# Optimization experiments

Measured on AMD Instinct MI355X. Metric: run time of the kernel, lower is better.

The kernel has to match this reference:

```python
import jax, jax.numpy as jnp
from jax import lax
import numpy as np

B = 32  # batch


def _conv(x, w, b, pad):
    # x: [B,Cin,H,W], w: [Cout,Cin,kh,kw], b: [Cout]
    y = lax.conv_general_dilated(x, w, window_strides=(1, 1), padding=pad,
                                 dimension_numbers=("NCHW", "OIHW", "NCHW"))
    return y + b[None, :, None, None]


def setup_inputs() -> dict:
    keys = jax.random.split(jax.random.key(0), 16)
    ki = iter(keys)
    f32 = jnp.float32

    def W(shape):
        return jax.random.normal(next(ki), shape, f32) * 0.05

    return {
        "x": jax.random.normal(next(ki), (B, 64, 64), f32),
        # 64 independent spatial convs per stage, each Conv2d(Cin,31,(64,3))
        "W1": W((64, 31, 1, 64, 3)),  "b1": jnp.zeros((64, 31), f32),
        "W2": W((64, 31, 31, 64, 3)), "b2": jnp.zeros((64, 31), f32),
        "W3": W((64, 31, 31, 64, 3)), "b3": jnp.zeros((64, 31), f32),
        # 2 edge spectral stacks: Conv(2,64,9)->ReLU->Conv(64,32,1)->ReLU->Conv(32,1,5)
        "We1a": W((2, 64, 2, 9, 9)),  "be1a": jnp.zeros((2, 64), f32),
        "We1b": W((2, 32, 64, 1, 1)), "be1b": jnp.zeros((2, 32), f32),
        "We1c": W((2, 1, 32, 5, 5)),  "be1c": jnp.zeros((2, 1), f32),
        # 29 interior spectral stacks: Conv(3,64,9)->ReLU->Conv(64,32,1)->ReLU->Conv(32,1,5)
        "We2a": W((29, 64, 3, 9, 9)),  "be2a": jnp.zeros((29, 64), f32),
        "We2b": W((29, 32, 64, 1, 1)), "be2b": jnp.zeros((29, 32), f32),
        "We2c": W((29, 1, 32, 5, 5)),  "be2c": jnp.zeros((29, 1), f32),
    }


def _spatial(inp, Ws, bs):
    # inp: [B,Cin,64,64]; Ws: [64,31,Cin,64,3]; bs: [64,31]
    def one(w, b):
        return jax.nn.relu(_conv(inp, w, b, [(0, 0), (1, 1)]))  # [B,31,1,64]
    rows = jax.vmap(one)(Ws, bs)            # [64,B,31,1,64]; row i = output line i
    return jnp.transpose(rows[:, :, :, 0, :], (1, 2, 0, 3))  # [B,31,64,64]


def _spectral(xin, wa, ba, wb, bb, wc, bc):
    h = jax.nn.relu(_conv(xin, wa, ba, [(4, 4), (4, 4)]))
    h = jax.nn.relu(_conv(h, wb, bb, [(0, 0), (0, 0)]))
    return _conv(h, wc, bc, [(2, 2), (2, 2)])[:, 0]  # [B,64,64]


def reference(x, W1, b1, W2, b2, W3, b3,
              We1a, be1a, We1b, be1b, We1c, be1c,
              We2a, be2a, We2b, be2b, We2c, be2c):
    xb = x[:, None]                         # [B,1,64,64]
    s1 = _spatial(xb, W1, b1)               # [B,31,64,64]
    s2 = _spatial(s1, W2, b2)
    s3 = _spatial(s2, W3, b3)

    # edge bands 0 and 30 use 2-channel slices
    edge_in = jnp.stack([s3[:, 0:2], s3[:, 29:31]])   # [2,B,2,64,64]
    edge = jax.vmap(_spectral)(edge_in, We1a, be1a, We1b, be1b, We1c, be1c)  # [2,B,64,64]

    # interior bands 1..29 use sliding 3-channel slices
    idx = jnp.arange(29)[:, None] + jnp.arange(3)[None, :]  # [29,3]
    mid_in = jnp.transpose(s3[:, idx], (1, 0, 2, 3, 4))     # [29,B,3,64,64]
    mid = jax.vmap(_spectral)(mid_in, We2a, be2a, We2b, be2b, We2c, be2c)  # [29,B,64,64]

    recon = jnp.concatenate(
        [edge[0][:, None], jnp.transpose(mid, (1, 0, 2, 3)), edge[1][:, None]], axis=1)
    out = s3 + recon                        # [B,31,64,64]
    # torch: .transpose(3,1).transpose(2,1) == permute(0,2,3,1)
    return jnp.transpose(out, (0, 2, 3, 1))  # [B,64,64,31]
```

## Files before the change

kernel.cpp:

```cpp
#include <hip/hip_runtime.h>
#include <hip/hip_bf16.h>
#include <stdint.h>

typedef unsigned short u16;
typedef unsigned int   u32;
typedef __attribute__((ext_vector_type(8))) short bf16x8;
typedef __attribute__((ext_vector_type(4))) float f32x4;

__device__ __forceinline__ float us2f(u16 u){ return __uint_as_float(((u32)u)<<16); }
__device__ __forceinline__ float lo2f(u32 w){ return __uint_as_float(w<<16); }
__device__ __forceinline__ float hi2f(u32 w){ return __uint_as_float(w & 0xffff0000u); }
__device__ __forceinline__ u16 f2us(float f){
  u32 u = __float_as_uint(f);
  u32 r = (u + 0x7FFFu + ((u>>16)&1u)) >> 16;
  return (u16)r;
}
__device__ __forceinline__ u32 pk2(float a, float b){ return (u32)f2us(a) | ((u32)f2us(b)<<16); }

__global__ __launch_bounds__(256) void k_prep_x(const float* __restrict__ x, u16* __restrict__ xT){
  __shared__ float tile[64][65];
  const int b = blockIdx.x, t = threadIdx.x;
  #pragma unroll
  for (int q=0;q<4;q++){
    int idx = q*256 + t, r = idx>>4, w4 = (idx&15)*4;
    float4 v = *(const float4*)&x[((size_t)b*64 + r)*64 + w4];
    tile[r][w4]=v.x; tile[r][w4+1]=v.y; tile[r][w4+2]=v.z; tile[r][w4+3]=v.w;
  }
  __syncthreads();
  #pragma unroll
  for (int q=0;q<2;q++){
    int idx = q*256 + t, w = idx>>3, rc = idx&7;
    uint4 o;
    o.x = pk2(tile[rc*8+0][w], tile[rc*8+1][w]);
    o.y = pk2(tile[rc*8+2][w], tile[rc*8+3][w]);
    o.z = pk2(tile[rc*8+4][w], tile[rc*8+5][w]);
    o.w = pk2(tile[rc*8+6][w], tile[rc*8+7][w]);
    *(uint4*)&xT[((size_t)b*64 + w)*64 + rc*8] = o;
  }
}

__global__ __launch_bounds__(256) void k_prep_w(const float* __restrict__ W,
        u16* __restrict__ Wp, int CI){
  __shared__ float rowW[5952];
  const int h = blockIdx.x, i = blockIdx.y, t = threadIdx.x;
  for (int idx=t; idx<1488; idx+=256){
    int o = idx/48, j4 = (idx - o*48)*4;
    float4 v = *(const float4*)&W[ (((size_t)h*31 + o)*CI + i)*192 + j4 ];
    *(float4*)&rowW[o*192 + j4] = v;
  }
  __syncthreads();
  for (int idx=t; idx<768; idx+=256){
    int dw = idx>>8, rem = idx&255, o = rem>>3, rc = rem&7;
    uint4 ov = {0,0,0,0};
    if (o < 31){
      const float* s = &rowW[o*192 + dw];
      ov.x = pk2(s[(rc*8+0)*3], s[(rc*8+1)*3]);
      ov.y = pk2(s[(rc*8+2)*3], s[(rc*8+3)*3]);
      ov.z = pk2(s[(rc*8+4)*3], s[(rc*8+5)*3]);
      ov.w = pk2(s[(rc*8+6)*3], s[(rc*8+7)*3]);
    }
    *(uint4*)&Wp[ ((((size_t)h*CI + i)*3 + dw)*32 + o)*64 + rc*8 ] = ov;
  }
}

__global__ __launch_bounds__(256) void k_tr(const u16* __restrict__ in, u16* __restrict__ outp){
  __shared__ u16 tile[64*72];
  const int b = blockIdx.x, o = blockIdx.y, t = threadIdx.x;
  const uint4* src = (const uint4*)(in + ((size_t)b*31 + o)*4096);
  #pragma unroll
  for (int q=0;q<2;q++){
    int idx = q*256 + t, hh = idx>>3, u = idx&7;
    *(uint4*)&tile[hh*72 + ((u ^ ((hh>>3)&7))*8)] = src[idx];
  }
  __syncthreads();
  u16* dst = outp + ((size_t)b*31 + o)*4096;
  #pragma unroll
  for (int q=0;q<2;q++){
    int idx = q*256 + t, w = idx>>3, hc = (idx&7)*8;
    u32 ow[4];
    #pragma unroll
    for (int j=0;j<4;j++){
      int h0 = hc + j*2, h1 = h0 + 1;
      u16 a = tile[h0*72 + (((w>>3) ^ ((h0>>3)&7))*8) + (w&7)];
      u16 bb= tile[h1*72 + (((w>>3) ^ ((h1>>3)&7))*8) + (w&7)];
      ow[j] = (u32)a | ((u32)bb<<16);
    }
    uint4 ov = {ow[0], ow[1], ow[2], ow[3]};
    *(uint4*)&dst[(size_t)w*64 + hc] = ov;
  }
}

__global__ __launch_bounds__(256) void k_spatial2(const u16* __restrict__ inT_g,
        const u16* __restrict__ Wp, const float* __restrict__ bias,
        float* __restrict__ outF, u16* __restrict__ outT, int CI, int mode){
  __shared__ __align__(16) u16 inT[2][66*72];
  const int t    = threadIdx.x;
  const int wv   = t>>6;
  const int lane = t&63;
  const int l15  = lane&15;
  const int quad = lane>>4;
  const int wg  = blockIdx.x;
  const int xcd = wg & 7;
  const int li  = wg >> 3;
  const int hg  = xcd*2 + (li>>5);
  const int b   = li & 31;
  const int h   = hg*4 + wv;

  if (t < 72){
    inT[0][t] = 0; inT[0][65*72 + t] = 0;
    inT[1][t] = 0; inT[1][65*72 + t] = 0;
  }

  f32x4 acc[2][4];
  #pragma unroll
  for (int n=0;n<2;n++)
    #pragma unroll
    for (int ms=0;ms<4;ms++) acc[n][ms] = (f32x4){0.f,0.f,0.f,0.f};

  const uint4* srcb = (const uint4*)(inT_g + (size_t)b*CI*4096);
  const u16*   wrow = Wp + (size_t)h*CI*3*32*64;

  uint4 pf[2];
  #pragma unroll
  for (int q=0;q<2;q++) pf[q] = srcb[q*256 + t];
  bf16x8 bA[2][3][2], bB[2][3][2];
  #pragma unroll
  for (int dw=0;dw<3;dw++)
    #pragma unroll
    for (int n=0;n<2;n++)
      #pragma unroll
      for (int kh=0;kh<2;kh++)
        bA[kh][dw][n] = *(const bf16x8*)&wrow[(dw*32 + n*16 + l15)*64 + kh*32 + quad*8];

  auto body = [&](bf16x8 (&bcur)[2][3][2], bf16x8 (&bnext)[2][3][2], int i){
    u16* L = inT[i&1];
    #pragma unroll
    for (int q=0;q<2;q++){
      int idx = q*256 + t, row = idx>>3, ch = idx&7;
      *(uint4*)&L[(row+1)*72 + ch*8] = pf[q];
    }
    int inext = (i+1 < CI) ? (i+1) : (CI-1);
    const uint4* src = srcb + (size_t)inext*512;
    #pragma unroll
    for (int q=0;q<2;q++) pf[q] = src[q*256 + t];
    const u16* wbase = wrow + (size_t)inext*3*32*64;
    #pragma unroll
    for (int dw=0;dw<3;dw++)
      #pragma unroll
      for (int n=0;n<2;n++)
        #pragma unroll
        for (int kh=0;kh<2;kh++)
          bnext[kh][dw][n] = *(const bf16x8*)&wbase[(dw*32 + n*16 + l15)*64 + kh*32 + quad*8];
    asm volatile("s_waitcnt lgkmcnt(0)" ::: "memory");
    __builtin_amdgcn_s_barrier();
    __builtin_amdgcn_sched_barrier(0);
    #pragma unroll
    for (int kh=0; kh<2; kh++){
      #pragma unroll
      for (int dw=0; dw<3; dw++){
        bf16x8 afr[4];
        #pragma unroll
        for (int ms=0;ms<4;ms++)
          afr[ms] = *(const bf16x8*)&L[(ms*16 + l15 + dw)*72 + kh*32 + quad*8];
        #pragma unroll
        for (int n=0;n<2;n++)
          #pragma unroll
          for (int ms=0;ms<4;ms++)
            acc[n][ms] = __builtin_amdgcn_mfma_f32_16x16x32_bf16(afr[ms], bcur[kh][dw][n], acc[n][ms], 0,0,0);
      }
    }
  };

  int i = 0;
  while (true){
    body(bA, bB, i); if (++i >= CI) break;
    body(bB, bA, i); if (++i >= CI) break;
  }

  #pragma unroll
  for (int n=0;n<2;n++){
    int o = n*16 + l15;
    if (o < 31){
      float bv = bias[h*31 + o];
      if (mode == 0){
        #pragma unroll
        for (int ms=0;ms<4;ms++){
          size_t base = (((size_t)b*31 + o)*64 + h)*64 + ms*16 + quad*4;
          #pragma unroll
          for (int reg=0;reg<4;reg++)
            outF[base + reg] = fmaxf(acc[n][ms][reg] + bv, 0.f);
        }
      } else {
        #pragma unroll
        for (int ms=0;ms<4;ms++){
          uint2 pw;
          pw.x = pk2(fmaxf(acc[n][ms][0] + bv, 0.f), fmaxf(acc[n][ms][1] + bv, 0.f));
          pw.y = pk2(fmaxf(acc[n][ms][2] + bv, 0.f), fmaxf(acc[n][ms][3] + bv, 0.f));
          *(uint2*)&outT[ (((size_t)b*31 + o)*64 + h)*64 + ms*16 + quad*4 ] = pw;
        }
      }
    }
  }
}

__global__ __launch_bounds__(256) void k_prep(
    const float* __restrict__ We1a, const float* __restrict__ We2a,
    const float* __restrict__ We1b, const float* __restrict__ We2b,
    u16* __restrict__ waP, u16* __restrict__ wbP){
  int t = blockIdx.x*256 + threadIdx.x;
  if (t < 17856){
    int g = t/576, rem = t - g*576, dx = rem>>6, c = rem&63;
    int C; const float* wa;
    if (g==0)      { C=2; wa = We1a; }
    else if (g==30){ C=2; wa = We1a + 64*2*81; }
    else           { C=3; wa = We2a + (size_t)(g-1)*64*3*81; }
    const float* wrow = wa + (size_t)c*C*81;
    u16* dst = waP + ((size_t)(g*9 + dx)*64 + c)*40;
    int Kr = C*9;
    for (int k=0;k<40;k++){
      u16 v = 0;
      if (k < Kr) v = f2us(wrow[k*9 + dx]);
      dst[k] = v;
    }
  } else if (t < 17856 + 992){
    int u = t - 17856; int g = u>>5, c2 = u&31;
    const float* wb;
    if (g==0)      wb = We1b;
    else if (g==30) wb = We1b + 32*64;
    else            wb = We2b + (size_t)(g-1)*32*64;
    u16* dst = wbP + ((size_t)g*32 + c2)*72;
    for (int k=0;k<64;k++) dst[k] = f2us(wb[c2*64 + k]);
    for (int k=64;k<72;k++) dst[k] = 0;
  }
}

__global__ __launch_bounds__(256) void k_spec_ab(
    const float* __restrict__ s3,
    const u16* __restrict__ waP, const u16* __restrict__ wbP,
    const float* __restrict__ be1a, const float* __restrict__ be1b,
    const float* __restrict__ be2a, const float* __restrict__ be2b,
    u16* __restrict__ hb, int g0){
  __shared__ __align__(16) unsigned char smem[36864];
  u16* colT = (u16*)smem;
  u16* haT  = (u16*)smem;
  u16* hbL  = (u16*)smem;

  const int t = threadIdx.x;
  const int yo = blockIdx.x, b = blockIdx.y;
  const int gl = blockIdx.z;
  const int g  = g0 + gl;
  const int y0 = yo*4;
  const int wv = t>>6, lane = t&63, l15 = lane&15, quad = lane>>4;

  int C, cb; const float *ba, *bb;
  if (g==0)      { C=2; cb=0;  ba=be1a;           bb=be1b;        }
  else if (g==30){ C=2; cb=29; ba=be1a+64;        bb=be1b+32;     }
  else           { C=3; cb=g-1; ba=be2a+(size_t)(g-1)*64; bb=be2b+(size_t)(g-1)*32; }

  {
    uint4 z = {0,0,0,0};
    uint4* c4 = (uint4*)colT;
    #pragma unroll
    for (int j=0;j<6;j++){ int idx = j*256 + t; if (idx < 1440) c4[idx] = z; }
  }
  __syncthreads();

  for (int idx=t; idx<576; idx+=256){
    int i = idx/192, rem = idx-192*i;
    int x4 = rem/12, yext = rem - x4*12;
    int yrow = y0 + yext - 4;
    if (i < C && yrow >= 0 && yrow < 64){
      float4 v = *(const float4*)&s3[ (((size_t)b*31 + cb + i)*64 + yrow)*64 + x4*4 ];
      u16 q0=f2us(v.x), q1=f2us(v.y), q2=f2us(v.z), q3=f2us(v.w);
      #pragma unroll
      for (int yl=0; yl<4; yl++){
        int dy = yext - yl;
        if (dy >= 0 && dy < 9){
          int k = i*9 + dy;
          int base = (yl*72 + x4*4 + 4)*40 + k;
          colT[base      ] = q0;
          colT[base + 40 ] = q1;
          colT[base + 80 ] = q2;
          colT[base + 120] = q3;
        }
      }
    }
  }
  __syncthreads();

  f32x4 acc[4][4];
  #pragma unroll
  for (int yl=0;yl<4;yl++)
    #pragma unroll
    for (int nf=0;nf<4;nf++) acc[yl][nf] = (f32x4){0.f,0.f,0.f,0.f};

  const u16* waPg = waP + (size_t)g*9*64*40;
  #pragma unroll
  for (int dx=0; dx<9; dx++){
    bf16x8 af[4];
    #pragma unroll
    for (int yl=0;yl<4;yl++)
      af[yl] = *(const bf16x8*)&colT[(yl*72 + wv*16 + l15 + dx)*40 + quad*8];
    #pragma unroll
    for (int nf=0;nf<4;nf++){
      bf16x8 bfr = *(const bf16x8*)&waPg[(dx*64 + nf*16 + l15)*40 + quad*8];
      #pragma unroll
      for (int yl=0;yl<4;yl++)
        acc[yl][nf] = __builtin_amdgcn_mfma_f32_16x16x32_bf16(af[yl], bfr, acc[yl][nf], 0,0,0);
    }
  }
  __syncthreads();

  #pragma unroll
  for (int nf=0;nf<4;nf++){
    float bav = ba[nf*16 + l15];
    #pragma unroll
    for (int yl=0;yl<4;yl++){
      int px = yl*64 + wv*16 + quad*4;
      #pragma unroll
      for (int reg=0;reg<4;reg++)
        haT[(px+reg)*72 + nf*16 + l15] = f2us(fmaxf(acc[yl][nf][reg] + bav, 0.f));
    }
  }
  __syncthreads();

  bf16x8 a2[2][4];
  #pragma unroll
  for (int kh=0; kh<2; kh++)
    #pragma unroll
    for (int j=0;j<4;j++)
      a2[kh][j] = *(const bf16x8*)&haT[((wv*4+j)*16 + l15)*72 + kh*32 + quad*8];
  __syncthreads();

  const u16* wb_g = wbP + (size_t)g*32*72;
  f32x4 acc2[4][2];
  #pragma unroll
  for (int j=0;j<4;j++){ acc2[j][0] = (f32x4){0.f,0.f,0.f,0.f}; acc2[j][1] = (f32x4){0.f,0.f,0.f,0.f}; }
  #pragma unroll
  for (int kh=0; kh<2; kh++){
    #pragma unroll
    for (int nf=0;nf<2;nf++){
      bf16x8 b2 = *(const bf16x8*)&wb_g[(nf*16 + l15)*72 + kh*32 + quad*8];
      #pragma unroll
      for (int j=0;j<4;j++)
        acc2[j][nf] = __builtin_amdgcn_mfma_f32_16x16x32_bf16(a2[kh][j], b2, acc2[j][nf], 0,0,0);
    }
  }
  #pragma unroll
  for (int nf=0;nf<2;nf++){
    float bbv = bb[nf*16 + l15];
    #pragma unroll
    for (int j=0;j<4;j++){
      int px = (wv*4+j)*16 + quad*4;
      uint2 pw;
      pw.x = pk2(fmaxf(acc2[j][nf][0] + bbv, 0.f), fmaxf(acc2[j][nf][1] + bbv, 0.f));
      pw.y = pk2(fmaxf(acc2[j][nf][2] + bbv, 0.f), fmaxf(acc2[j][nf][3] + bbv, 0.f));
      *(uint2*)&hbL[(nf*16+l15)*296 + px] = pw;
    }
  }
  __syncthreads();

  {
    int c2 = t>>3, xq = t&7;
    size_t base = (((size_t)gl*32 + b)*32 + c2)*4096 + (size_t)yo*256 + xq*32;
    #pragma unroll
    for (int q=0;q<4;q++)
      *(uint4*)&hb[base + q*8] = *(const uint4*)&hbL[c2*296 + xq*32 + q*8];
  }
}

__global__ __launch_bounds__(256) void k_spec_c(
    const u16* __restrict__ hb, const float* __restrict__ We1c, const float* __restrict__ be1c,
    const float* __restrict__ We2c, const float* __restrict__ be2c,
    float* __restrict__ rec, int g0){
  __shared__ __align__(16) unsigned char smemC[58368 + 3200];
  u16*   hbT  = (u16*)smemC;
  float* wcL  = (float*)(smemC + 58368);
  float* redc = (float*)smemC;
  const int t  = threadIdx.x;
  const int y0 = blockIdx.x*8;
  const int b  = blockIdx.y;
  const int gl = blockIdx.z;
  const int g  = g0 + gl;
  const float *wc, *bc;
  if (g==0)      { wc = We1c;             bc = be1c;       }
  else if (g==30){ wc = We1c + 800;       bc = be1c + 1;   }
  else           { wc = We2c + (g-1)*800; bc = be2c + (g-1); }

  for (int idx=t; idx<384; idx+=256){
    int c2 = idx/12, row = idx - c2*12;
    u32* d32 = (u32*)&hbT[(size_t)(c2*12 + row)*76];
    d32[0]  = 0;
    d32[33] = 0;
    u32* di = d32 + 1;
    int yg = y0 - 2 + row;
    if (yg >= 0 && yg < 64){
      const uint4* srcp = (const uint4*)&hb[ (((size_t)gl*32 + b)*32 + c2)*4096 + (size_t)yg*64 ];
      #pragma unroll
      for (int q=0;q<8;q++){
        uint4 v = srcp[q];
        di[q*4+0]=v.x; di[q*4+1]=v.y; di[q*4+2]=v.z; di[q*4+3]=v.w;
      }
    } else {
      #pragma unroll
      for (int q=0;q<32;q++) di[q] = 0;
    }
  }
  for (int idx=t; idx<800; idx+=256) wcL[idx] = wc[idx];
  __syncthreads();

  const int xt = t&7, yq = (t>>3)&7, cqt = t>>6;
  const int x0 = xt*8;
  float acc[8];
  #pragma unroll
  for (int p=0;p<8;p++) acc[p]=0.f;
  for (int c2 = cqt*8; c2 < cqt*8+8; c2++){
    #pragma unroll
    for (int dy=0;dy<5;dy++){
      const uint2* hp = (const uint2*)&hbT[(c2*12 + yq+dy)*76 + x0];
      uint2 v0 = hp[0], v1 = hp[1], v2 = hp[2];
      float h[12];
      h[0]=lo2f(v0.x); h[1]=hi2f(v0.x); h[2]=lo2f(v0.y); h[3]=hi2f(v0.y);
      h[4]=lo2f(v1.x); h[5]=hi2f(v1.x); h[6]=lo2f(v1.y); h[7]=hi2f(v1.y);
      h[8]=lo2f(v2.x); h[9]=hi2f(v2.x); h[10]=lo2f(v2.y); h[11]=hi2f(v2.y);
      #pragma unroll
      for (int dx=0;dx<5;dx++){
        float wv = wcL[c2*25 + dy*5 + dx];
        #pragma unroll
        for (int p=0;p<8;p++) acc[p] = fmaf(h[p+dx], wv, acc[p]);
      }
    }
  }
  __syncthreads();
  int slot = yq*8 + xt;
  if (cqt >= 2){
    #pragma unroll
    for (int p=0;p<8;p++) redc[((cqt-2)*64 + slot)*8 + p] = acc[p];
  }
  __syncthreads();
  if (cqt < 2){
    #pragma unroll
    for (int p=0;p<8;p++) acc[p] += redc[(cqt*64 + slot)*8 + p];
  }
  __syncthreads();
  if (cqt == 1){
    #pragma unroll
    for (int p=0;p<8;p++) redc[slot*8 + p] = acc[p];
  }
  __syncthreads();
  if (cqt == 0){
    float bcv = bc[0];
    size_t base = (((size_t)g*32 + b)*64 + (y0+yq))*64 + x0;
    #pragma unroll
    for (int p=0;p<8;p++) rec[base+p] = acc[p] + redc[slot*8 + p] + bcv;
  }
}

__global__ __launch_bounds__(256) void k_final(const float* __restrict__ s3,
        const float* __restrict__ rec, float* __restrict__ out){
  __shared__ float tile[31][65];
  const int t = threadIdx.x;
  const int y = blockIdx.x & 63;
  const int b = blockIdx.x >> 6;
  for (int idx=t; idx<1984; idx+=256){
    int o = idx>>6, x = idx&63;
    tile[o][x] = s3[ (((size_t)b*31+o)*64 + y)*64 + x ]
               + rec[ (((size_t)o*32+b)*64 + y)*64 + x ];
  }
  __syncthreads();
  size_t base = ((size_t)b*4096 + (size_t)y*64)*31;
  for (int idx=t; idx<1984; idx+=256){
    int x = idx/31, o = idx-31*x;
    out[base+idx] = tile[o][x];
  }
}

extern "C" void kernel_launch(void* const* d_in, const int* in_sizes, int n_in,
                              void* d_out, int out_size, void* d_ws, size_t ws_size,
                              hipStream_t stream){
  const float* x    = (const float*)d_in[0];
  const float* W1   = (const float*)d_in[1];
  const float* b1   = (const float*)d_in[2];
  const float* W2   = (const float*)d_in[3];
  const float* b2   = (const float*)d_in[4];
  const float* W3   = (const float*)d_in[5];
  const float* b3   = (const float*)d_in[6];
  const float* We1a = (const float*)d_in[7];
  const float* be1a = (const float*)d_in[8];
  const float* We1b = (const float*)d_in[9];
  const float* be1b = (const float*)d_in[10];
  const float* We1c = (const float*)d_in[11];
  const float* be1c = (const float*)d_in[12];
  const float* We2a = (const float*)d_in[13];
  const float* be2a = (const float*)d_in[14];
  const float* We2b = (const float*)d_in[15];
  const float* be2b = (const float*)d_in[16];
  const float* We2c = (const float*)d_in[17];
  const float* be2c = (const float*)d_in[18];
  float* out = (float*)d_out;

  char* ws = (char*)d_ws;
  float* s3  = (float*)(ws);
  u16*   Wp  = (u16*)(ws + 16777216);
  u16*   xT  = (u16*)(ws + 44040192);
  float* rec = (float*)(ws + 16777216);
  u16*   hb  = (u16*)(ws + 33030144);

  u16* bufA = (u16*)((char*)d_out);
  u16* bufB = (u16*)((char*)d_out + 8126464);
  u16* waP = (u16*)((char*)d_out);
  u16* wbP = (u16*)((char*)d_out + 1440000);

  dim3 bs(256);
  dim3 gsp(512), gtr(32,31);
  k_prep_x<<<dim3(32),bs,0,stream>>>(x, xT);
  k_prep_w<<<dim3(64,1),bs,0,stream>>>(W1, Wp, 1);
  k_spatial2<<<gsp,bs,0,stream>>>(xT,  Wp, b1, nullptr, bufA, 1, 1);
  k_tr<<<gtr,bs,0,stream>>>(bufA, bufB);
  k_prep_w<<<dim3(64,31),bs,0,stream>>>(W2, Wp, 31);
  k_spatial2<<<gsp,bs,0,stream>>>(bufB, Wp, b2, nullptr, bufA, 31, 1);
  k_tr<<<gtr,bs,0,stream>>>(bufA, bufB);
  k_prep_w<<<dim3(64,31),bs,0,stream>>>(W3, Wp, 31);
  k_spatial2<<<gsp,bs,0,stream>>>(bufB, Wp, b3, s3, nullptr, 31, 0);

  k_prep<<<dim3(74),bs,0,stream>>>(We1a, We2a, We1b, We2b, waP, wbP);

  int batch = 8;
  if (ws_size > 33030144ull){
    size_t m = (ws_size - 33030144ull) / 8388608ull;
    if (m < 1) m = 1;
    if (m > 8) m = 8;
    batch = (int)m;
  }
  for (int g0=0; g0<31; g0+=batch){
    int c = 31 - g0; if (c > batch) c = batch;
    k_spec_ab<<<dim3(16,32,c),bs,0,stream>>>(s3, waP, wbP, be1a, be1b, be2a, be2b, hb, g0);
    k_spec_c <<<dim3(8,32,c),bs,0,stream>>>(hb, We1c,be1c,We2c,be2c, rec, g0);
  }
  k_final<<<dim3(2048),bs,0,stream>>>(s3, rec, out);
}
```

Before: 994.5 us.

## Split spatial conv work per wave over half-width tiles with private LDS

Each workgroup of the spatial conv kernel now covers 2 output rows times 2 half-width column halves, one per wave, and the grid doubles to 1024 blocks. Each wave stages its own 34-row halo slice in a private LDS buffer, so the block-wide barrier and the double-buffered weight prefetch go away. Weight fragments are now loaded per kh right before use, and launch bounds request 4 blocks per CU. The aim is more parallelism and occupancy with fewer registers and less sync. In exchange, weight loads are exposed, adjacent waves reload overlapping halo rows, and the kernel relies on LDS reads completing without an explicit wait between the store and the MFMA loads.

```diff
diff --git a/kernel.cpp b/kernel.cpp
--- a/kernel.cpp
+++ b/kernel.cpp
@@ -90,10 +90,10 @@
   }
 }
 
-__global__ __launch_bounds__(256) void k_spatial2(const u16* __restrict__ inT_g,
+__global__ __launch_bounds__(256, 4) void k_spatial2(const u16* __restrict__ inT_g,
         const u16* __restrict__ Wp, const float* __restrict__ bias,
         float* __restrict__ outF, u16* __restrict__ outT, int CI, int mode){
-  __shared__ __align__(16) u16 inT[2][66*72];
+  __shared__ __align__(16) u16 S[4][34*72];
   const int t    = threadIdx.x;
   const int wv   = t>>6;
   const int lane = t&63;
@@ -102,79 +102,79 @@
   const int wg  = blockIdx.x;
   const int xcd = wg & 7;
   const int li  = wg >> 3;
-  const int hg  = xcd*2 + (li>>5);
+  const int hp  = li >> 5;
   const int b   = li & 31;
-  const int h   = hg*4 + wv;
-
-  if (t < 72){
-    inT[0][t] = 0; inT[0][65*72 + t] = 0;
-    inT[1][t] = 0; inT[1][65*72 + t] = 0;
-  }
-
-  f32x4 acc[2][4];
+  const int h   = xcd*8 + hp*2 + (wv&1);
+  const int wh  = wv >> 1;
+  const int w0  = wh*32;
+
+  u16* L = S[wv];
+
+  f32x4 acc[2][2];
   #pragma unroll
   for (int n=0;n<2;n++)
     #pragma unroll
-    for (int ms=0;ms<4;ms++) acc[n][ms] = (f32x4){0.f,0.f,0.f,0.f};
+    for (int ms=0;ms<2;ms++) acc[n][ms] = (f32x4){0.f,0.f,0.f,0.f};
 
   const uint4* srcb = (const uint4*)(inT_g + (size_t)b*CI*4096);
   const u16*   wrow = Wp + (size_t)h*CI*3*32*64;
 
-  uint4 pf[2];
-  #pragma unroll
-  for (int q=0;q<2;q++) pf[q] = srcb[q*256 + t];
-  bf16x8 bA[2][3][2], bB[2][3][2];
-  #pragma unroll
-  for (int dw=0;dw<3;dw++)
-    #pragma unroll
-    for (int n=0;n<2;n++)
-      #pragma unroll
-      for (int kh=0;kh<2;kh++)
-        bA[kh][dw][n] = *(const bf16x8*)&wrow[(dw*32 + n*16 + l15)*64 + kh*32 + quad*8];
-
-  auto body = [&](bf16x8 (&bcur)[2][3][2], bf16x8 (&bnext)[2][3][2], int i){
-    u16* L = inT[i&1];
-    #pragma unroll
-    for (int q=0;q<2;q++){
-      int idx = q*256 + t, row = idx>>3, ch = idx&7;
-      *(uint4*)&L[(row+1)*72 + ch*8] = pf[q];
-    }
-    int inext = (i+1 < CI) ? (i+1) : (CI-1);
-    const uint4* src = srcb + (size_t)inext*512;
-    #pragma unroll
-    for (int q=0;q<2;q++) pf[q] = src[q*256 + t];
-    const u16* wbase = wrow + (size_t)inext*3*32*64;
-    #pragma unroll
-    for (int dw=0;dw<3;dw++)
-      #pragma unroll
-      for (int n=0;n<2;n++)
+  uint4 pf[5];
+  const uint4 zz = {0,0,0,0};
+
+  auto issue_pf = [&](int ch){
+    const uint4* src = srcb + (size_t)ch*512;
+    #pragma unroll
+    for (int k=0;k<4;k++){
+      int c = lane + 64*k, row = c>>3, cn = c&7;
+      int gw = w0 - 1 + row;
+      pf[k] = zz;
+      if (gw >= 0 && gw < 64) pf[k] = src[gw*8 + cn];
+    }
+    {
+      int c = 256 + lane, row = c>>3, cn = c&7;
+      int gw = w0 - 1 + row;
+      pf[4] = zz;
+      if (lane < 16 && gw >= 0 && gw < 64) pf[4] = src[gw*8 + cn];
+    }
+  };
+
+  issue_pf(0);
+
+  for (int i=0;i<CI;i++){
+    #pragma unroll
+    for (int k=0;k<4;k++){
+      int c = lane + 64*k, row = c>>3, cn = c&7;
+      *(uint4*)&L[row*72 + cn*8] = pf[k];
+    }
+    if (lane < 16){
+      int c = 256 + lane, row = c>>3, cn = c&7;
+      *(uint4*)&L[row*72 + cn*8] = pf[4];
+    }
+    if (i+1 < CI) issue_pf(i+1);
+
+    const u16* wbase = wrow + (size_t)i*6144;
+    #pragma unroll
+    for (int kh=0; kh<2; kh++){
+      bf16x8 bfrk[3][2];
+      #pragma unroll
+      for (int dw=0;dw<3;dw++)
         #pragma unroll
-        for (int kh=0;kh<2;kh++)
-          bnext[kh][dw][n] = *(const bf16x8*)&wbase[(dw*32 + n*16 + l15)*64 + kh*32 + quad*8];
-    asm volatile("s_waitcnt lgkmcnt(0)" ::: "memory");
-    __builtin_amdgcn_s_barrier();
-    __builtin_amdgcn_sched_barrier(0);
-    #pragma unroll
-    for (int kh=0; kh<2; kh++){
+        for (int n=0;n<2;n++)
+          bfrk[dw][n] = *(const bf16x8*)&wbase[(dw*32 + n*16 + l15)*64 + kh*32 + quad*8];
       #pragma unroll
       for (int dw=0; dw<3; dw++){
-        bf16x8 afr[4];
+        bf16x8 afr[2];
         #pragma unroll
-        for (int ms=0;ms<4;ms++)
+        for (int ms=0;ms<2;ms++)
           afr[ms] = *(const bf16x8*)&L[(ms*16 + l15 + dw)*72 + kh*32 + quad*8];
         #pragma unroll
         for (int n=0;n<2;n++)
           #pragma unroll
-          for (int ms=0;ms<4;ms++)
-            acc[n][ms] = __builtin_amdgcn_mfma_f32_16x16x32_bf16(afr[ms], bcur[kh][dw][n], acc[n][ms], 0,0,0);
+          for (int ms=0;ms<2;ms++)
+            acc[n][ms] = __builtin_amdgcn_mfma_f32_16x16x32_bf16(afr[ms], bfrk[dw][n], acc[n][ms], 0,0,0);
       }
     }
-  };
-
-  int i = 0;
-  while (true){
-    body(bA, bB, i); if (++i >= CI) break;
-    body(bB, bA, i); if (++i >= CI) break;
   }
 
   #pragma unroll
@@ -184,19 +184,19 @@
       float bv = bias[h*31 + o];
       if (mode == 0){
         #pragma unroll
-        for (int ms=0;ms<4;ms++){
-          size_t base = (((size_t)b*31 + o)*64 + h)*64 + ms*16 + quad*4;
+        for (int ms=0;ms<2;ms++){
+          size_t base = (((size_t)b*31 + o)*64 + h)*64 + w0 + ms*16 + quad*4;
           #pragma unroll
           for (int reg=0;reg<4;reg++)
             outF[base + reg] = fmaxf(acc[n][ms][reg] + bv, 0.f);
         }
       } else {
         #pragma unroll
-        for (int ms=0;ms<4;ms++){
+        for (int ms=0;ms<2;ms++){
           uint2 pw;
           pw.x = pk2(fmaxf(acc[n][ms][0] + bv, 0.f), fmaxf(acc[n][ms][1] + bv, 0.f));
           pw.y = pk2(fmaxf(acc[n][ms][2] + bv, 0.f), fmaxf(acc[n][ms][3] + bv, 0.f));
-          *(uint2*)&outT[ (((size_t)b*31 + o)*64 + h)*64 + ms*16 + quad*4 ] = pw;
+          *(uint2*)&outT[ (((size_t)b*31 + o)*64 + h)*64 + w0 + ms*16 + quad*4 ] = pw;
         }
       }
     }
@@ -512,7 +512,7 @@
   u16* wbP = (u16*)((char*)d_out + 1440000);
 
   dim3 bs(256);
-  dim3 gsp(512), gtr(32,31);
+  dim3 gsp(1024), gtr(32,31);
   k_prep_x<<<dim3(32),bs,0,stream>>>(x, xT);
   k_prep_w<<<dim3(64,1),bs,0,stream>>>(W1, Wp, 1);
   k_spatial2<<<gsp,bs,0,stream>>>(xT,  Wp, b1, nullptr, bufA, 1, 1);
```

Result: slower. 1.132 ms (+13.9%).

## Retile spatial conv blocks to 2 rows × 2 batches per workgroup

Applied to the files above, without the earlier changes.

Each workgroup of k_spatial2 now covers 2 output rows for 2 batch samples instead of 4 rows for 1 sample. It stages two input images per channel in a doubled shared-memory buffer and raises launch bounds to request 2 blocks per CU. This changes the balance of reuse: weights are shared across batches within a block, while input tiles are reused across fewer rows. The aim is better weight reuse and occupancy, at the cost of more LDS and more input loads per thread.

```diff
diff --git a/kernel.cpp b/kernel.cpp
--- a/kernel.cpp
+++ b/kernel.cpp
@@ -90,10 +90,10 @@
   }
 }
 
-__global__ __launch_bounds__(256) void k_spatial2(const u16* __restrict__ inT_g,
+__global__ __launch_bounds__(256, 2) void k_spatial2(const u16* __restrict__ inT_g,
         const u16* __restrict__ Wp, const float* __restrict__ bias,
         float* __restrict__ outF, u16* __restrict__ outT, int CI, int mode){
-  __shared__ __align__(16) u16 inT[2][66*72];
+  __shared__ __align__(16) u16 S[2][2][66*72];
   const int t    = threadIdx.x;
   const int wv   = t>>6;
   const int lane = t&63;
@@ -102,13 +102,16 @@
   const int wg  = blockIdx.x;
   const int xcd = wg & 7;
   const int li  = wg >> 3;
-  const int hg  = xcd*2 + (li>>5);
-  const int b   = li & 31;
-  const int h   = hg*4 + wv;
+  const int hq  = xcd*4 + (li>>4);
+  const int bg  = li & 15;
+  const int hl  = wv & 1;
+  const int bl  = wv >> 1;
+  const int h   = hq*2 + hl;
+  const int b   = bg*2 + bl;
 
   if (t < 72){
-    inT[0][t] = 0; inT[0][65*72 + t] = 0;
-    inT[1][t] = 0; inT[1][65*72 + t] = 0;
+    int zbl = t/36, rem = t - zbl*36, zdb = rem/18, r2 = (rem%18)/9, j = rem%9;
+    *(uint4*)&S[zbl][zdb][(r2 ? 65*72 : 0) + j*8] = (uint4){0,0,0,0};
   }
 
   f32x4 acc[2][4];
@@ -117,12 +120,18 @@
     #pragma unroll
     for (int ms=0;ms<4;ms++) acc[n][ms] = (f32x4){0.f,0.f,0.f,0.f};
 
-  const uint4* srcb = (const uint4*)(inT_g + (size_t)b*CI*4096);
-  const u16*   wrow = Wp + (size_t)h*CI*3*32*64;
-
-  uint4 pf[2];
-  #pragma unroll
-  for (int q=0;q<2;q++) pf[q] = srcb[q*256 + t];
+  const uint4* srcb0 = (const uint4*)(inT_g + (size_t)((bg*2+0)*CI)*4096);
+  const uint4* srcb1 = (const uint4*)(inT_g + (size_t)((bg*2+1)*CI)*4096);
+  const u16*   wrow  = Wp + (size_t)h*CI*3*32*64;
+
+  uint4 pf[4];
+  #pragma unroll
+  for (int k=0;k<4;k++){
+    int u = k*256 + t;
+    int sbl = u>>9, c = u&511;
+    const uint4* src = sbl ? srcb1 : srcb0;
+    pf[k] = src[c];
+  }
   bf16x8 bA[2][3][2], bB[2][3][2];
   #pragma unroll
   for (int dw=0;dw<3;dw++)
@@ -133,17 +142,20 @@
         bA[kh][dw][n] = *(const bf16x8*)&wrow[(dw*32 + n*16 + l15)*64 + kh*32 + quad*8];
 
   auto body = [&](bf16x8 (&bcur)[2][3][2], bf16x8 (&bnext)[2][3][2], int i){
-    u16* L = inT[i&1];
-    #pragma unroll
-    for (int q=0;q<2;q++){
-      int idx = q*256 + t, row = idx>>3, ch = idx&7;
-      *(uint4*)&L[(row+1)*72 + ch*8] = pf[q];
+    #pragma unroll
+    for (int k=0;k<4;k++){
+      int u = k*256 + t, sbl = u>>9, c = u&511;
+      int row = c>>3, cn = c&7;
+      *(uint4*)&S[sbl][i&1][(row+1)*72 + cn*8] = pf[k];
     }
     int inext = (i+1 < CI) ? (i+1) : (CI-1);
-    const uint4* src = srcb + (size_t)inext*512;
-    #pragma unroll
-    for (int q=0;q<2;q++) pf[q] = src[q*256 + t];
-    const u16* wbase = wrow + (size_t)inext*3*32*64;
+    #pragma unroll
+    for (int k=0;k<4;k++){
+      int u = k*256 + t, sbl = u>>9, c = u&511;
+      const uint4* src = (sbl ? srcb1 : srcb0) + (size_t)inext*512;
+      pf[k] = src[c];
+    }
+    const u16* wbase = wrow + (size_t)inext*6144;
     #pragma unroll
     for (int dw=0;dw<3;dw++)
       #pragma unroll
@@ -154,6 +166,7 @@
     asm volatile("s_waitcnt lgkmcnt(0)" ::: "memory");
     __builtin_amdgcn_s_barrier();
     __builtin_amdgcn_sched_barrier(0);
+    const u16* L = S[bl][i&1];
     #pragma unroll
     for (int kh=0; kh<2; kh++){
       #pragma unroll
```

Measured after the change: 1.040 ms. +4.5%, slower.
